# Optimization experiments

Hardware: AMD Instinct MI355X
Metric: run time of the kernel (lower is better)

Reference implementation:

```python
import jax, jax.numpy as jnp
import numpy as np

H = 768          # hidden_size
NH = 12          # num_attention_heads
DH = H // NH     # attention_head_size = 64
NE_TYPES = 16    # num_edge_types
B, S = 4, 512
N = B * S        # flattened node count
E = 131072       # number of edges


def setup_inputs() -> dict:
    key = jax.random.key(0)
    ks = jax.random.split(key, 12)
    inp = {
        "hidden_states": jax.random.normal(ks[0], (B, S, H), dtype=jnp.float32),
        "Wq": jax.random.normal(ks[1], (H, H), dtype=jnp.float32) * 0.02,
        "bq": jnp.zeros((H,), dtype=jnp.float32),
        "Wk": jax.random.normal(ks[2], (H, H), dtype=jnp.float32) * 0.02,
        "bk": jnp.zeros((H,), dtype=jnp.float32),
        "Wv": jax.random.normal(ks[3], (H, H), dtype=jnp.float32) * 0.02,
        "bv": jnp.zeros((H,), dtype=jnp.float32),
        "rel_key_emb": jax.random.normal(ks[4], (NE_TYPES, DH), dtype=jnp.float32) * 0.02,
        "rel_val_emb": jax.random.normal(ks[5], (NE_TYPES, DH), dtype=jnp.float32) * 0.02,
        "edges_src": jax.random.randint(ks[6], (E,), 0, N, dtype=jnp.int32),
        "edges_tgt": jax.random.randint(ks[7], (E,), 0, N, dtype=jnp.int32),
        "edges_type": jax.random.randint(ks[8], (E,), 0, NE_TYPES, dtype=jnp.int32),
        "edges_pos": jax.random.randint(ks[9], (E,), 0, NE_TYPES, dtype=jnp.int32),
    }
    return inp


def reference(hidden_states, Wq, bq, Wk, bk, Wv, bv, rel_key_emb, rel_val_emb,
              edges_src, edges_tgt, edges_type, edges_pos):
    b, s, h = hidden_states.shape
    n = b * s
    hs = hidden_states.reshape(n, h)
    # Q/K/V projections, split into heads: [N, NH, DH]
    q = (hs @ Wq.T + bq).reshape(n, NH, DH)
    k = (hs @ Wk.T + bk).reshape(n, NH, DH)
    v = (hs @ Wv.T + bv).reshape(n, NH, DH)
    # Edge gather + relative key embedding (broadcast over heads)
    src_key = k[edges_src] + rel_key_emb[edges_pos][:, None, :]      # [E, NH, DH]
    tgt_query = q[edges_tgt]                                          # [E, NH, DH]
    # Unnormalized exp attention scores per edge per head: [E, NH]
    scores = jnp.exp(jnp.sum(tgt_query * src_key, axis=-1) / jnp.sqrt(jnp.float32(DH)))
    # Segment softmax normalization via scatter-add over target nodes
    denom = jax.ops.segment_sum(scores, edges_tgt, num_segments=n)    # [N, NH]
    attn = scores / denom[edges_tgt]                                  # [E, NH]
    # Reweighted per-edge values (the meaningful computed quantity)
    src_val = v[edges_src] + rel_val_emb[edges_pos][:, None, :]       # [E, NH, DH]
    weighted = src_val * attn[:, :, None]                             # [E, NH, DH]
    # NOTE: the original torch forward returns hidden_states unchanged
    # (the attention chain is dead code). We return the computed edge-weighted
    # values as the correctness target for the gather->exp->scatter-softmax chain.
    return weighted
```

## Files before the change

kernel.cpp:

```cpp
#include <hip/hip_runtime.h>
#include <hip/hip_bf16.h>

#define H 768
#define NH 12
#define DH 64
#define NNODES 2048
#define NEDGES 131072

typedef __bf16 bf16x8 __attribute__((ext_vector_type(8)));
typedef float floatx4 __attribute__((ext_vector_type(4)));

#define GLOAD_LDS16(gptr, ldsptr)                                                        \
  __builtin_amdgcn_global_load_lds((const __attribute__((address_space(1))) void*)(gptr), \
                                   (__attribute__((address_space(3))) void*)(ldsptr),     \
                                   16, 0, 0)

__device__ __forceinline__ unsigned short f2bf(float x) {
  union { __hip_bfloat16 h; unsigned short u; } cv;
  cv.h = __float2bfloat16(x);
  return cv.u;
}

__global__ __launch_bounds__(256)
void convert_kernel(const float* __restrict__ hs,
                    const float* __restrict__ Wq,
                    const float* __restrict__ Wk,
                    const float* __restrict__ Wv,
                    __hip_bfloat16* __restrict__ hsb,
                    __hip_bfloat16* __restrict__ wb,
                    int* __restrict__ hist) {
  int i = blockIdx.x * 256 + threadIdx.x;
  const int n_hs4 = NNODES * H / 4;
  const int n_w4  = H * H / 4;
  if (i < n_hs4) {
    float4 v = ((const float4*)hs)[i];
    ((ushort4*)hsb)[i] = make_ushort4(f2bf(v.x), f2bf(v.y), f2bf(v.z), f2bf(v.w));
    return;
  }
  int j = i - n_hs4;
  if (j < 3 * n_w4) {
    const float* src = (j < n_w4) ? Wq : (j < 2 * n_w4 ? Wk : Wv);
    float4 v = ((const float4*)src)[j % n_w4];
    ((ushort4*)wb)[j] = make_ushort4(f2bf(v.x), f2bf(v.y), f2bf(v.z), f2bf(v.w));
    return;
  }
  int z = j - 3 * n_w4;
  if (z < NNODES / 4) {
    ((int4*)hist)[z] = make_int4(0, 0, 0, 0);
  }
}

__global__ __launch_bounds__(256)
void qkv_gemm(const __hip_bfloat16* __restrict__ A,
              const __hip_bfloat16* __restrict__ Wb,
              const float* __restrict__ b0,
              const float* __restrict__ b1,
              const float* __restrict__ b2,
              float* __restrict__ out) {
  __shared__ __hip_bfloat16 As[128][32];
  __shared__ __hip_bfloat16 Bs[128][32];

  const int t    = threadIdx.x;
  const int wave = t >> 6;
  const int lane = t & 63;
  const int bm   = blockIdx.x * 128;
  const int bn   = blockIdx.y * 128;
  const int mat  = blockIdx.z;

  const __hip_bfloat16* B = Wb + (size_t)mat * H * H;
  const float* bias = (mat == 0) ? b0 : ((mat == 1) ? b1 : b2);
  float* C = out + (size_t)mat * NNODES * H;

  const int wm = (wave & 1) * 64;
  const int wn = (wave >> 1) * 64;
  const int lr = lane & 15;
  const int lq = lane >> 4;

  floatx4 acc[4][4] = {};

  const int ar = t >> 2;
  const int ac = (t & 3) * 8;
  __hip_bfloat16* AsF = &As[0][0];
  __hip_bfloat16* BsF = &Bs[0][0];

  for (int kt = 0; kt < H; kt += 32) {
    GLOAD_LDS16(A + (size_t)(bm + ar) * H + kt + ac,      AsF + t * 8);
    GLOAD_LDS16(A + (size_t)(bm + 64 + ar) * H + kt + ac, AsF + 64 * 32 + t * 8);
    GLOAD_LDS16(B + (size_t)(bn + ar) * H + kt + ac,      BsF + t * 8);
    GLOAD_LDS16(B + (size_t)(bn + 64 + ar) * H + kt + ac, BsF + 64 * 32 + t * 8);
    __syncthreads();

    bf16x8 af[4], bfr[4];
#pragma unroll
    for (int i = 0; i < 4; i++)
      af[i] = *(const bf16x8*)&As[wm + i * 16 + lr][lq * 8];
#pragma unroll
    for (int i = 0; i < 4; i++)
      bfr[i] = *(const bf16x8*)&Bs[wn + i * 16 + lr][lq * 8];
#pragma unroll
    for (int mi = 0; mi < 4; mi++)
#pragma unroll
      for (int ni = 0; ni < 4; ni++)
        acc[mi][ni] = __builtin_amdgcn_mfma_f32_16x16x32_bf16(
            af[mi], bfr[ni], acc[mi][ni], 0, 0, 0);
    __syncthreads();
  }

#pragma unroll
  for (int ni = 0; ni < 4; ni++) {
    int col = bn + wn + ni * 16 + lr;
    float bv = bias[col];
#pragma unroll
    for (int mi = 0; mi < 4; mi++) {
#pragma unroll
      for (int r = 0; r < 4; r++) {
        int row = bm + wm + mi * 16 + lq * 4 + r;
        C[(size_t)row * H + col] = acc[mi][ni][r] + bv;
      }
    }
  }
}

__global__ __launch_bounds__(256)
void hist_kernel(const int* __restrict__ etgt, int* __restrict__ hist) {
  int e = blockIdx.x * 256 + threadIdx.x;
  atomicAdd(&hist[etgt[e]], 1);
}

__global__ __launch_bounds__(256)
void scan_kernel(const int* __restrict__ hist, int* __restrict__ rowptr,
                 int* __restrict__ cursor) {
  __shared__ int part[256];
  int t = threadIdx.x;
  int loc[8];
  int s = 0;
#pragma unroll
  for (int k = 0; k < 8; k++) { loc[k] = s; s += hist[t * 8 + k]; }
  part[t] = s;
  __syncthreads();
  for (int off = 1; off < 256; off <<= 1) {
    int v = (t >= off) ? part[t - off] : 0;
    __syncthreads();
    if (t >= off) part[t] += v;
    __syncthreads();
  }
  int pre = part[t] - s;
#pragma unroll
  for (int k = 0; k < 8; k++) {
    rowptr[t * 8 + k] = pre + loc[k];
    cursor[t * 8 + k] = pre + loc[k];
  }
  if (t == 255) rowptr[NNODES] = part[255];
}

__global__ __launch_bounds__(256)
void scatter_kernel(const int* __restrict__ esrc, const int* __restrict__ etgt,
                    const int* __restrict__ epos,
                    int* __restrict__ cursor,
                    int* __restrict__ src_s, int* __restrict__ pos_s,
                    int* __restrict__ einv) {
  int e = blockIdx.x * 256 + threadIdx.x;
  int tgt = etgt[e];
  int slot = atomicAdd(&cursor[tgt], 1);
  src_s[slot] = esrc[e];
  pos_s[slot] = epos[e];
  einv[e] = slot;
}

__global__ __launch_bounds__(256)
void scores3_kernel(const float* __restrict__ Q, const float* __restrict__ K,
                    const float* __restrict__ relk,
                    const int* __restrict__ rowptr,
                    const int* __restrict__ src_s, const int* __restrict__ pos_s,
                    float* __restrict__ scores_s, float* __restrict__ denom) {
  const int t    = blockIdx.x;
  const int tid  = threadIdx.x;
  const int wave = tid >> 6;
  const int lane = tid & 63;
  const int g    = lane >> 4;
  const int off  = (lane & 15) * 4;

  __shared__ float Qs[H];
  __shared__ float Rk[16 * DH];
  __shared__ float dpart[4][NH];

  if (tid < 192)
    *(float4*)&Qs[tid * 4] = *(const float4*)(Q + (size_t)t * H + tid * 4);
  *(float4*)&Rk[tid * 4] = *(const float4*)(relk + tid * 4);
  __syncthreads();

  const int beg = rowptr[t], end = rowptr[t + 1];
  float dacc0 = 0.f, dacc1 = 0.f, dacc2 = 0.f;

  for (int i = beg + wave; i < end; i += 4) {
    const int src = src_s[i];
    const int pos = pos_s[i];
    const float* Kp = K + (size_t)src * H;
    const float4 r4 = *(const float4*)&Rk[pos * DH + off];
    float s[3];
#pragma unroll
    for (int c = 0; c < 3; c++) {
      float4 k4 = *(const float4*)(Kp + c * 256 + lane * 4);
      float4 q4 = *(const float4*)&Qs[c * 256 + lane * 4];
      s[c] = q4.x * (k4.x + r4.x) + q4.y * (k4.y + r4.y) +
             q4.z * (k4.z + r4.z) + q4.w * (k4.w + r4.w);
    }
#pragma unroll
    for (int m = 1; m < 16; m <<= 1) {
      s[0] += __shfl_xor(s[0], m);
      s[1] += __shfl_xor(s[1], m);
      s[2] += __shfl_xor(s[2], m);
    }
    if ((lane & 15) == 0) {
      float sc0 = __expf(s[0] * 0.125f);
      float sc1 = __expf(s[1] * 0.125f);
      float sc2 = __expf(s[2] * 0.125f);
      scores_s[(size_t)i * NH + g]     = sc0;
      scores_s[(size_t)i * NH + 4 + g] = sc1;
      scores_s[(size_t)i * NH + 8 + g] = sc2;
      dacc0 += sc0; dacc1 += sc1; dacc2 += sc2;
    }
  }

  if ((lane & 15) == 0) {
    dpart[wave][g]     = dacc0;
    dpart[wave][4 + g] = dacc1;
    dpart[wave][8 + g] = dacc2;
  }
  __syncthreads();
  if (tid < NH) {
    denom[(size_t)t * NH + tid] =
        dpart[0][tid] + dpart[1][tid] + dpart[2][tid] + dpart[3][tid];
  }
}

__global__ __launch_bounds__(256)
void weighted_kernel(const float* __restrict__ V, const float* __restrict__ relv,
                     const int* __restrict__ esrc, const int* __restrict__ etgt,
                     const int* __restrict__ epos,
                     const int* __restrict__ einv,
                     const float* __restrict__ scores_s,
                     const float* __restrict__ denom,
                     float* __restrict__ out) {
  const int wave = threadIdx.x >> 6;
  const int lane = threadIdx.x & 63;
  const int e = blockIdx.x * 4 + wave;
  const int src = esrc[e], tgt = etgt[e], pos = epos[e];
  const int sidx = einv[e];
  const int g = lane >> 4;
  const int off = (lane & 15) * 4;

  const float4 r4 = *(const float4*)(relv + pos * DH + off);
#pragma unroll
  for (int c = 0; c < 3; c++) {
    int h = c * 4 + g;
    float a = scores_s[(size_t)sidx * NH + h] / denom[(size_t)tgt * NH + h];
    float4 v4 = *(const float4*)(V + (size_t)src * H + c * 256 + lane * 4);
    floatx4 o;
    o.x = (v4.x + r4.x) * a;
    o.y = (v4.y + r4.y) * a;
    o.z = (v4.z + r4.z) * a;
    o.w = (v4.w + r4.w) * a;
    __builtin_nontemporal_store(o, (floatx4*)(out + (size_t)e * H + c * 256 + lane * 4));
  }
}

extern "C" void kernel_launch(void* const* d_in, const int* in_sizes, int n_in,
                              void* d_out, int out_size, void* d_ws, size_t ws_size,
                              hipStream_t stream) {
  const float* hs   = (const float*)d_in[0];
  const float* Wq   = (const float*)d_in[1];
  const float* bq   = (const float*)d_in[2];
  const float* Wk   = (const float*)d_in[3];
  const float* bk   = (const float*)d_in[4];
  const float* Wv   = (const float*)d_in[5];
  const float* bv   = (const float*)d_in[6];
  const float* relk = (const float*)d_in[7];
  const float* relv = (const float*)d_in[8];
  const int* esrc   = (const int*)d_in[9];
  const int* etgt   = (const int*)d_in[10];
  const int* epos   = (const int*)d_in[12];
  float* out = (float*)d_out;

  char* ws = (char*)d_ws;
  __hip_bfloat16* hsb = (__hip_bfloat16*)ws;
  __hip_bfloat16* wb  = (__hip_bfloat16*)(ws + 3145728);
  float* qkv      = (float*)(ws + 6684672);
  float* scores_s = (float*)(ws + 25559040);
  float* denom    = (float*)(ws + 31850496);
  int* hist       = (int*)(ws + 31948800);
  int* rowptr     = (int*)(ws + 31956992);
  int* cursor     = (int*)(ws + 31965200);
  int* src_s = (int*)ws;
  int* pos_s = (int*)(ws + 524288);
  int* einv  = (int*)(ws + 1048576);

  convert_kernel<<<3266, 256, 0, stream>>>(hs, Wq, Wk, Wv, hsb, wb, hist);

  dim3 grid_gemm(16, 6, 3);
  qkv_gemm<<<grid_gemm, 256, 0, stream>>>(hsb, wb, bq, bk, bv, qkv);

  const float* Qp = qkv;
  const float* Kp = qkv + (size_t)NNODES * H;
  const float* Vp = qkv + (size_t)2 * NNODES * H;

  hist_kernel<<<NEDGES / 256, 256, 0, stream>>>(etgt, hist);
  scan_kernel<<<1, 256, 0, stream>>>(hist, rowptr, cursor);
  scatter_kernel<<<NEDGES / 256, 256, 0, stream>>>(esrc, etgt, epos, cursor,
                                                   src_s, pos_s, einv);

  scores3_kernel<<<NNODES, 256, 0, stream>>>(Qp, Kp, relk, rowptr, src_s, pos_s,
                                             scores_s, denom);

  weighted_kernel<<<NEDGES / 4, 256, 0, stream>>>(Vp, relv, esrc, etgt, epos,
                                                  einv, scores_s, denom, out);
}
```

Measured before the change: 537.3 us.

## Store K projection in bf16 for score gathers and shrink GEMM tiles

The QKV GEMM now writes the K matrix as bf16 into a separate workspace buffer, and the score kernel gathers K rows as bf16 and widens them to float in registers. This halves the bytes fetched per edge gather in the score kernel. The GEMM tile also shrinks from 128x128 to 64x64 to launch more blocks across the CUs. The cost is extra rounding error in the scores and less data reuse per GEMM block.

```diff
diff --git a/kernel.cpp b/kernel.cpp
--- a/kernel.cpp
+++ b/kernel.cpp
@@ -19,6 +19,12 @@
   union { __hip_bfloat16 h; unsigned short u; } cv;
   cv.h = __float2bfloat16(x);
   return cv.u;
+}
+
+__device__ __forceinline__ float bfu2f(unsigned short u) {
+  union { float f; unsigned int i; } c;
+  c.i = ((unsigned int)u) << 16;
+  return c.f;
 }
 
 __global__ __launch_bounds__(256)
@@ -56,27 +62,27 @@
               const float* __restrict__ b0,
               const float* __restrict__ b1,
               const float* __restrict__ b2,
-              float* __restrict__ out) {
-  __shared__ __hip_bfloat16 As[128][32];
-  __shared__ __hip_bfloat16 Bs[128][32];
+              float* __restrict__ out,
+              __hip_bfloat16* __restrict__ kb) {
+  __shared__ __hip_bfloat16 As[64][32];
+  __shared__ __hip_bfloat16 Bs[64][32];
 
   const int t    = threadIdx.x;
   const int wave = t >> 6;
   const int lane = t & 63;
-  const int bm   = blockIdx.x * 128;
-  const int bn   = blockIdx.y * 128;
+  const int bm   = blockIdx.x * 64;
+  const int bn   = blockIdx.y * 64;
   const int mat  = blockIdx.z;
 
   const __hip_bfloat16* B = Wb + (size_t)mat * H * H;
   const float* bias = (mat == 0) ? b0 : ((mat == 1) ? b1 : b2);
-  float* C = out + (size_t)mat * NNODES * H;
-
-  const int wm = (wave & 1) * 64;
-  const int wn = (wave >> 1) * 64;
+
+  const int wm = (wave & 1) * 32;
+  const int wn = (wave >> 1) * 32;
   const int lr = lane & 15;
   const int lq = lane >> 4;
 
-  floatx4 acc[4][4] = {};
+  floatx4 acc[2][2] = {};
 
   const int ar = t >> 2;
   const int ac = (t & 3) * 8;
@@ -84,38 +90,53 @@
   __hip_bfloat16* BsF = &Bs[0][0];
 
   for (int kt = 0; kt < H; kt += 32) {
-    GLOAD_LDS16(A + (size_t)(bm + ar) * H + kt + ac,      AsF + t * 8);
-    GLOAD_LDS16(A + (size_t)(bm + 64 + ar) * H + kt + ac, AsF + 64 * 32 + t * 8);
-    GLOAD_LDS16(B + (size_t)(bn + ar) * H + kt + ac,      BsF + t * 8);
-    GLOAD_LDS16(B + (size_t)(bn + 64 + ar) * H + kt + ac, BsF + 64 * 32 + t * 8);
+    GLOAD_LDS16(A + (size_t)(bm + ar) * H + kt + ac, AsF + t * 8);
+    GLOAD_LDS16(B + (size_t)(bn + ar) * H + kt + ac, BsF + t * 8);
     __syncthreads();
 
-    bf16x8 af[4], bfr[4];
-#pragma unroll
-    for (int i = 0; i < 4; i++)
+    bf16x8 af[2], bfr[2];
+#pragma unroll
+    for (int i = 0; i < 2; i++)
       af[i] = *(const bf16x8*)&As[wm + i * 16 + lr][lq * 8];
 #pragma unroll
-    for (int i = 0; i < 4; i++)
+    for (int i = 0; i < 2; i++)
       bfr[i] = *(const bf16x8*)&Bs[wn + i * 16 + lr][lq * 8];
 #pragma unroll
-    for (int mi = 0; mi < 4; mi++)
-#pragma unroll
-      for (int ni = 0; ni < 4; ni++)
+    for (int mi = 0; mi < 2; mi++)
+#pragma unroll
+      for (int ni = 0; ni < 2; ni++)
         acc[mi][ni] = __builtin_amdgcn_mfma_f32_16x16x32_bf16(
             af[mi], bfr[ni], acc[mi][ni], 0, 0, 0);
     __syncthreads();
   }
 
-#pragma unroll
-  for (int ni = 0; ni < 4; ni++) {
-    int col = bn + wn + ni * 16 + lr;
-    float bv = bias[col];
-#pragma unroll
-    for (int mi = 0; mi < 4; mi++) {
-#pragma unroll
-      for (int r = 0; r < 4; r++) {
-        int row = bm + wm + mi * 16 + lq * 4 + r;
-        C[(size_t)row * H + col] = acc[mi][ni][r] + bv;
+  if (mat == 1) {
+#pragma unroll
+    for (int ni = 0; ni < 2; ni++) {
+      int col = bn + wn + ni * 16 + lr;
+      float bv = bias[col];
+#pragma unroll
+      for (int mi = 0; mi < 2; mi++) {
+#pragma unroll
+        for (int r = 0; r < 4; r++) {
+          int row = bm + wm + mi * 16 + lq * 4 + r;
+          kb[(size_t)row * H + col] = __float2bfloat16(acc[mi][ni][r] + bv);
+        }
+      }
+    }
+  } else {
+    float* C = out + (size_t)mat * NNODES * H;
+#pragma unroll
+    for (int ni = 0; ni < 2; ni++) {
+      int col = bn + wn + ni * 16 + lr;
+      float bv = bias[col];
+#pragma unroll
+      for (int mi = 0; mi < 2; mi++) {
+#pragma unroll
+        for (int r = 0; r < 4; r++) {
+          int row = bm + wm + mi * 16 + lq * 4 + r;
+          C[(size_t)row * H + col] = acc[mi][ni][r] + bv;
+        }
       }
     }
   }
@@ -168,7 +189,8 @@
 }
 
 __global__ __launch_bounds__(256)
-void scores3_kernel(const float* __restrict__ Q, const float* __restrict__ K,
+void scores3_kernel(const float* __restrict__ Q,
+                    const __hip_bfloat16* __restrict__ Kb,
                     const float* __restrict__ relk,
                     const int* __restrict__ rowptr,
                     const int* __restrict__ src_s, const int* __restrict__ pos_s,
@@ -195,15 +217,15 @@
   for (int i = beg + wave; i < end; i += 4) {
     const int src = src_s[i];
     const int pos = pos_s[i];
-    const float* Kp = K + (size_t)src * H;
+    const unsigned short* Kp = (const unsigned short*)(Kb + (size_t)src * H);
     const float4 r4 = *(const float4*)&Rk[pos * DH + off];
     float s[3];
 #pragma unroll
     for (int c = 0; c < 3; c++) {
-      float4 k4 = *(const float4*)(Kp + c * 256 + lane * 4);
+      ushort4 ku = *(const ushort4*)(Kp + c * 256 + lane * 4);
       float4 q4 = *(const float4*)&Qs[c * 256 + lane * 4];
-      s[c] = q4.x * (k4.x + r4.x) + q4.y * (k4.y + r4.y) +
-             q4.z * (k4.z + r4.z) + q4.w * (k4.w + r4.w);
+      s[c] = q4.x * (bfu2f(ku.x) + r4.x) + q4.y * (bfu2f(ku.y) + r4.y) +
+             q4.z * (bfu2f(ku.z) + r4.z) + q4.w * (bfu2f(ku.w) + r4.w);
     }
 #pragma unroll
     for (int m = 1; m < 16; m <<= 1) {
@@ -291,17 +313,17 @@
   int* hist       = (int*)(ws + 31948800);
   int* rowptr     = (int*)(ws + 31956992);
   int* cursor     = (int*)(ws + 31965200);
+  __hip_bfloat16* kb = (__hip_bfloat16*)(ws + 31973392);
   int* src_s = (int*)ws;
   int* pos_s = (int*)(ws + 524288);
   int* einv  = (int*)(ws + 1048576);
 
   convert_kernel<<<3266, 256, 0, stream>>>(hs, Wq, Wk, Wv, hsb, wb, hist);
 
-  dim3 grid_gemm(16, 6, 3);
-  qkv_gemm<<<grid_gemm, 256, 0, stream>>>(hsb, wb, bq, bk, bv, qkv);
+  dim3 grid_gemm(32, 12, 3);
+  qkv_gemm<<<grid_gemm, 256, 0, stream>>>(hsb, wb, bq, bk, bv, qkv, kb);
 
   const float* Qp = qkv;
-  const float* Kp = qkv + (size_t)NNODES * H;
   const float* Vp = qkv + (size_t)2 * NNODES * H;
 
   hist_kernel<<<NEDGES / 256, 256, 0, stream>>>(etgt, hist);
@@ -309,7 +331,7 @@
   scatter_kernel<<<NEDGES / 256, 256, 0, stream>>>(esrc, etgt, epos, cursor,
                                                    src_s, pos_s, einv);
 
-  scores3_kernel<<<NNODES, 256, 0, stream>>>(Qp, Kp, relk, rowptr, src_s, pos_s,
+  scores3_kernel<<<NNODES, 256, 0, stream>>>(Qp, kb, relk, rowptr, src_s, pos_s,
                                              scores_s, denom);
 
   weighted_kernel<<<NEDGES / 4, 256, 0, stream>>>(Vp, relv, esrc, etgt, epos,
```

Measured after the change: 529.8 us. No clear change (-1.4%).
